# Kernel tuning notes

Hardware: AMD Instinct MI355X
Metric: run time of the kernel (lower is better)

## Reference

```python
import jax, jax.numpy as jnp
import numpy as np

# dims
BS = 4096
MOVE = 4
N_EN, ED = 64, 16
N_AL, AD = 63, 16
OTHER = 20
MF = MOVE + OTHER            # m_f_size = 24
IN = MOVE + N_EN * ED + N_AL * AD + OTHER  # 2056
H = 4                        # n_head
HE = 128                     # hypernet_emb
E = 64                       # attention_dim (emb_dim)
NA = N_EN + N_AL + 1         # n_agents = 128
RNN = 256
EN_START = MOVE
AL_START = MOVE + N_EN * ED
OTH_START = AL_START + N_AL * AD


def setup_inputs() -> dict:
    key = jax.random.key(0)
    ks = jax.random.split(key, 32)
    g = lambda k, shape: (jax.random.normal(k, shape, dtype=jnp.float32) * 0.05)
    return {
        "obs": jax.random.normal(ks[0], (BS, IN), dtype=jnp.float32),
        # per-head query MLP (Linear(MF,HE)+ReLU+Linear(HE,E,no bias)), stacked over heads
        "Wq1": g(ks[1], (H, HE, MF)), "bq1": g(ks[2], (H, HE)), "Wq2": g(ks[3], (H, E, HE)),
        # per-head key_m MLP
        "Wkm1": g(ks[4], (H, HE, MF)), "bkm1": g(ks[5], (H, HE)), "Wkm2": g(ks[6], (H, E, HE)),
        # per-head entity key linears (no bias)
        "Wke": g(ks[7], (H, E, ED)), "Wka": g(ks[8], (H, E, AD)),
        # per-head value_m MLP
        "Wvm1": g(ks[9], (H, HE, MF)), "bvm1": g(ks[10], (H, HE)), "Wvm2": g(ks[11], (H, E, HE)),
        # per-head entity value linears (no bias)
        "Wve": g(ks[12], (H, E, ED)), "Wva": g(ks[13], (H, E, AD)),
        # b net: Linear(IN,E)+ReLU+Linear(E,1)
        "Wb1": g(ks[14], (E, IN)), "bb1": g(ks[15], (E,)), "Wb2": g(ks[16], (1, E)), "bb2": g(ks[17], (1,)),
        # hyper_w_head: Linear(IN,HE)+ReLU+Linear(HE,H)
        "Wh1": g(ks[18], (HE, IN)), "bh1": g(ks[19], (HE,)), "Wh2": g(ks[20], (H, HE)), "bh2": g(ks[21], (H,)),
        # final layer: Linear(E*NA, RNN)
        "Wf": g(ks[22], (RNN, E * NA)), "bf": g(ks[23], (RNN,)),
    }


def _headed_mlp(x, W1, b1, W2):
    # x: [B, MF]; W1: [H, HE, MF]; W2: [H, E, HE] -> [B, H, E]
    h = jax.nn.relu(jnp.einsum("bf,hgf->bhg", x, W1) + b1[None])
    return jnp.einsum("bhg,heg->bhe", h, W2)


def reference(obs, Wq1, bq1, Wq2, Wkm1, bkm1, Wkm2, Wke, Wka,
              Wvm1, bvm1, Wvm2, Wve, Wva, Wb1, bb1, Wb2, bb2,
              Wh1, bh1, Wh2, bh2, Wf, bf):
    bs = obs.shape[0]
    m = jnp.concatenate([obs[:, :MOVE], obs[:, OTH_START:]], axis=1)        # [B, MF]
    enemies = obs[:, EN_START:AL_START].reshape(bs, N_EN, ED)               # [B, N_EN, ED]
    allies = obs[:, AL_START:OTH_START].reshape(bs, N_AL, AD)               # [B, N_AL, AD]

    q = _headed_mlp(m, Wq1, bq1, Wq2)                                       # [B, H, E]
    km = _headed_mlp(m, Wkm1, bkm1, Wkm2)[:, :, None, :]                    # [B, H, 1, E]
    ke = jnp.einsum("bnd,hed->bhne", enemies, Wke)                          # [B, H, N_EN, E]
    ka = jnp.einsum("bnd,hed->bhne", allies, Wka)                           # [B, H, N_AL, E]
    k = jnp.concatenate([km, ke, ka], axis=2)                               # [B, H, NA, E]

    vm = _headed_mlp(m, Wvm1, bvm1, Wvm2)[:, :, None, :]
    ve = jnp.einsum("bnd,hed->bhne", enemies, Wve)
    va = jnp.einsum("bnd,hed->bhne", allies, Wva)
    v = jnp.concatenate([vm, ve, va], axis=2)                               # [B, H, NA, E]

    logits = jnp.einsum("bhe,bhne->bhn", q, k) / np.sqrt(E).astype(np.float32)
    w = jax.nn.softmax(logits, axis=-1)                                     # [B, H, NA]
    # torch: atten_w (B,1,NA) expanded to (B,E,NA) * v permuted to (B,E,NA); flatten [E,NA]
    scores = (w[:, :, None, :] * jnp.swapaxes(v, 2, 3)).reshape(bs, H, E * NA)

    b_term = jax.nn.relu(obs @ Wb1.T + bb1) @ Wb2.T + bb2                   # [B, 1]
    w_head = jnp.abs(jax.nn.relu(obs @ Wh1.T + bh1) @ Wh2.T + bh2)          # [B, H]
    mixed = jnp.einsum("bhk,bh->bk", scores, w_head) + b_term               # [B, E*NA]
    return mixed @ Wf.T + bf                                                # [B, RNN]
```

## Files before the change

kernel.cpp:

```cpp
#include <hip/hip_runtime.h>
#include <hip/hip_bf16.h>

typedef __attribute__((ext_vector_type(8))) short short8;
typedef __attribute__((ext_vector_type(4))) float floatx4;

#define NIN 2056
#define KPAD 2080
#define NBS 4096

__device__ __forceinline__ void gl_lds16(const ushort* g, ushort* l) {
#if defined(__has_builtin) && __has_builtin(__builtin_amdgcn_global_load_lds)
  __builtin_amdgcn_global_load_lds(
      (const __attribute__((address_space(1))) unsigned int*)g,
      (__attribute__((address_space(3))) unsigned int*)l, 16, 0, 0);
#else
  *(uint4*)l = *(const uint4*)g;
#endif
}

__device__ __forceinline__ float wsum(float v) {
#pragma unroll
  for (int o = 32; o; o >>= 1) v += __shfl_xor(v, o, 64);
  return v;
}
__device__ __forceinline__ float wmax(float v) {
#pragma unroll
  for (int o = 32; o; o >>= 1) v = fmaxf(v, __shfl_xor(v, o, 64));
  return v;
}

__global__ void prep_small(const float* __restrict__ obs,
                           const float* __restrict__ Wb1, const float* __restrict__ Wh1,
                           const float* __restrict__ Wq1, const float* __restrict__ Wkm1,
                           const float* __restrict__ Wvm1, const float* __restrict__ bq1,
                           const float* __restrict__ bkm1, const float* __restrict__ bvm1,
                           const float* __restrict__ Wq2, const float* __restrict__ Wkm2,
                           const float* __restrict__ Wvm2,
                           __hip_bfloat16* __restrict__ mmat,
                           __hip_bfloat16* __restrict__ w1cat,
                           __hip_bfloat16* __restrict__ w1m, float* __restrict__ b1cat,
                           __hip_bfloat16* __restrict__ w2cat) {
  int bid = blockIdx.x, tid = threadIdx.x;
  if (bid < 512) {
    int idx = bid * 256 + tid;
    int b = idx >> 5, j = idx & 31;
    float v = 0.f;
    if (j < 4) v = obs[(size_t)b * NIN + j];
    else if (j < 24) v = obs[(size_t)b * NIN + 2032 + j];
    mmat[idx] = __float2bfloat16(v);
  } else if (bid < 704) {
    int r = bid - 512;
    const float* src = (r < 64) ? (Wb1 + (size_t)r * NIN) : (Wh1 + (size_t)(r - 64) * NIN);
    for (int j = tid; j < KPAD; j += 256)
      w1cat[(size_t)r * KPAD + j] = __float2bfloat16(j < NIN ? src[j] : 0.f);
  } else if (bid < 896) {
    int idx = (bid - 704) * 256 + tid;
    int row = idx >> 5, j = idx & 31;
    int net = row >> 9, hg = row & 511;
    const float* W1 = net == 0 ? Wq1 : (net == 1 ? Wkm1 : Wvm1);
    float v = (j < 24) ? W1[(size_t)hg * 24 + j] : 0.f;
    w1m[idx] = __float2bfloat16(v);
    if (j == 0) {
      const float* b1 = net == 0 ? bq1 : (net == 1 ? bkm1 : bvm1);
      b1cat[row] = b1[hg];
    }
  } else {
    int idx = (bid - 896) * 256 + tid;
    int row = idx >> 7, g = idx & 127;
    int net = row >> 8, he = row & 255;
    const float* W2 = net == 0 ? Wq2 : (net == 1 ? Wkm2 : Wvm2);
    w2cat[idx] = __float2bfloat16(W2[(size_t)he * 128 + g]);
  }
}

__global__ void p6a_twf(const float* __restrict__ Wf, float* __restrict__ Wft,
                        float* __restrict__ rowsum) {
  __shared__ float t[64][65];
  int kt = blockIdx.x, rt = blockIdx.y;
  int tid = threadIdx.x;
  int kl = tid & 63, r0 = tid >> 6;
#pragma unroll
  for (int ii = 0; ii < 16; ++ii) {
    int rl = ii * 4 + r0;
    t[rl][kl] = Wf[(size_t)(rt * 64 + rl) * 8192 + kt * 64 + kl];
  }
  __syncthreads();
#pragma unroll
  for (int ii = 0; ii < 16; ++ii) {
    int kl2 = ii * 4 + r0;
    Wft[(size_t)(kt * 64 + kl2) * 256 + rt * 64 + kl] = t[kl][kl2];
  }
  if (tid < 64) {
    float s = 0.f;
    for (int kk = 0; kk < 64; ++kk) s += t[tid][kk];
    atomicAdd(&rowsum[rt * 64 + tid], s);
  }
}

__global__ void p6b_yt(const float* __restrict__ Wft, const float* __restrict__ Wve,
                       const float* __restrict__ Wva, __hip_bfloat16* __restrict__ Yt) {
  int n = blockIdx.x;
  int r = threadIdx.x;
  if (n == 0) {
    alignas(16) __hip_bfloat16 tmp[8];
    for (int e0 = 0; e0 < 64; e0 += 8) {
#pragma unroll
      for (int j = 0; j < 8; ++j)
        tmp[j] = __float2bfloat16(Wft[(size_t)((e0 + j) * 128) * 256 + r]);
      *(uint4*)(Yt + (size_t)r * 8192 + 8128 + e0) = *(const uint4*)tmp;
    }
    return;
  }
  const float* Wv = (n <= 64) ? Wve : Wva;
  float accv[64];
#pragma unroll
  for (int j = 0; j < 64; ++j) accv[j] = 0.f;
  for (int e = 0; e < 64; ++e) {
    float v = Wft[(size_t)(e * 128 + n) * 256 + r];
#pragma unroll
    for (int hd = 0; hd < 64; ++hd)
      accv[hd] += Wv[(hd >> 4) * 1024 + e * 16 + (hd & 15)] * v;
  }
#pragma unroll
  for (int c = 0; c < 8; ++c) {
    alignas(16) __hip_bfloat16 tmp[8];
#pragma unroll
    for (int j = 0; j < 8; ++j) tmp[j] = __float2bfloat16(accv[c * 8 + j]);
    *(uint4*)(Yt + (size_t)r * 8192 + (n - 1) * 64 + c * 8) = *(const uint4*)tmp;
  }
}

template <bool BIAS_RELU_BF16>
__global__ __launch_bounds__(256) void gemm64(
    const __hip_bfloat16* __restrict__ A, int lda, long aZ,
    const __hip_bfloat16* __restrict__ B, int ldb, long bZ,
    float* __restrict__ Cf, __hip_bfloat16* __restrict__ Cb, int ldc, long cZ,
    int nK, const float* __restrict__ bias) {
  __shared__ alignas(16) ushort lA[64 * 40];
  __shared__ alignas(16) ushort lB[64 * 40];
  int mt = blockIdx.x, nt = blockIdx.y, z = blockIdx.z;
  const ushort* Ag = (const ushort*)A + (size_t)z * aZ + (size_t)mt * 64 * lda;
  const ushort* Bg = (const ushort*)B + (size_t)z * bZ + (size_t)nt * 64 * ldb;
  int t = threadIdx.x;
  int w = t >> 6, l = t & 63, r16 = l & 15, kg = l >> 4;
  int srow = t >> 2, skc = (t & 3) * 8;
  const ushort* ga = Ag + (size_t)srow * lda + skc;
  const ushort* gb = Bg + (size_t)srow * ldb + skc;
  ushort* sa = lA + srow * 40 + skc;
  ushort* sb = lB + srow * 40 + skc;
  const ushort* fa = lA + (w * 16 + r16) * 40 + kg * 8;
  const ushort* fb0 = lB + r16 * 40 + kg * 8;
  floatx4 zero4 = {0.f, 0.f, 0.f, 0.f};
  floatx4 acc[4] = {zero4, zero4, zero4, zero4};
  for (int ks = 0; ks < nK; ++ks) {
    uint4 va = *(const uint4*)(ga + ks * 32);
    uint4 vb = *(const uint4*)(gb + ks * 32);
    __syncthreads();
    *(uint4*)sa = va;
    *(uint4*)sb = vb;
    __syncthreads();
    short8 a = *(const short8*)fa;
#pragma unroll
    for (int c = 0; c < 4; ++c) {
      short8 bb = *(const short8*)(fb0 + c * 16 * 40);
      acc[c] = __builtin_amdgcn_mfma_f32_16x16x32_bf16(a, bb, acc[c], 0, 0, 0);
    }
  }
  int row0 = mt * 64 + w * 16 + kg * 4;
  int col0 = nt * 64 + r16;
#pragma unroll
  for (int c = 0; c < 4; ++c) {
    int col = col0 + c * 16;
#pragma unroll
    for (int r = 0; r < 4; ++r) {
      int row = row0 + r;
      float v = acc[c][r];
      if (BIAS_RELU_BF16) {
        v += bias[col];
        v = v > 0.f ? v : 0.f;
        Cb[(size_t)z * cZ + (size_t)row * ldc + col] = __float2bfloat16(v);
      } else {
        Cf[(size_t)z * cZ + (size_t)row * ldc + col] = v;
      }
    }
  }
}

__global__ __launch_bounds__(256) void gemm_h1(
    const float* __restrict__ obs, const __hip_bfloat16* __restrict__ w1cat_,
    float* __restrict__ H1p) {
  __shared__ alignas(16) ushort lA[64 * 40];
  __shared__ alignas(16) ushort lB[64 * 40];
  const ushort* w1cat = (const ushort*)w1cat_;
  int mt = blockIdx.x, nt = blockIdx.y, z = blockIdx.z;
  int t = threadIdx.x;
  int w = t >> 6, l = t & 63, r16 = l & 15, kg = l >> 4;
  int srow = t >> 2, sc = (t & 3) * 8;
  int k0 = z * 512;
  const float* ga = obs + (size_t)(mt * 64 + srow) * NIN + k0 + sc;
  const ushort* gb = w1cat + (size_t)(nt * 64 + srow) * KPAD + k0 + sc;
  ushort* sa = lA + srow * 40 + sc;
  ushort* sb = lB + srow * 40 + sc;
  const ushort* fa = lA + (w * 16 + r16) * 40 + kg * 8;
  const ushort* fb0 = lB + r16 * 40 + kg * 8;
  floatx4 zero4 = {0.f, 0.f, 0.f, 0.f};
  floatx4 acc[4] = {zero4, zero4, zero4, zero4};
  int nK = (z == 3) ? 17 : 16;
  for (int ks = 0; ks < nK; ++ks) {
    float4 f0, f1;
    uint4 vb;
    bool tail = (ks == 16);
    if (!tail || (t & 3) == 0) {
      f0 = *(const float4*)(ga + ks * 32);
      f1 = *(const float4*)(ga + ks * 32 + 4);
    } else {
      f0 = make_float4(0.f, 0.f, 0.f, 0.f);
      f1 = make_float4(0.f, 0.f, 0.f, 0.f);
    }
    vb = *(const uint4*)(gb + ks * 32);
    __syncthreads();
    alignas(16) __hip_bfloat16 tmp[8];
    tmp[0] = __float2bfloat16(f0.x); tmp[1] = __float2bfloat16(f0.y);
    tmp[2] = __float2bfloat16(f0.z); tmp[3] = __float2bfloat16(f0.w);
    tmp[4] = __float2bfloat16(f1.x); tmp[5] = __float2bfloat16(f1.y);
    tmp[6] = __float2bfloat16(f1.z); tmp[7] = __float2bfloat16(f1.w);
    *(uint4*)sa = *(const uint4*)tmp;
    *(uint4*)sb = vb;
    __syncthreads();
    short8 a = *(const short8*)fa;
#pragma unroll
    for (int c = 0; c < 4; ++c) {
      short8 bb = *(const short8*)(fb0 + c * 16 * 40);
      acc[c] = __builtin_amdgcn_mfma_f32_16x16x32_bf16(a, bb, acc[c], 0, 0, 0);
    }
  }
  int row0 = mt * 64 + w * 16 + kg * 4;
  int col0 = nt * 64 + r16;
  float* C = H1p + (size_t)z * NBS * 192;
#pragma unroll
  for (int c = 0; c < 4; ++c)
#pragma unroll
    for (int r = 0; r < 4; ++r)
      C[(size_t)(row0 + r) * 192 + col0 + c * 16] = acc[c][r];
}

__global__ __launch_bounds__(256) void gemm_final(
    const ushort* __restrict__ Xg, const ushort* __restrict__ Yt,
    float* __restrict__ part) {
  __shared__ alignas(16) ushort lA[128 * 32];
  __shared__ alignas(16) ushort lB[128 * 32];
  int bid = blockIdx.x;
  int z = bid & 7, nt = (bid >> 3) & 1, mt = bid >> 4;
  int t = threadIdx.x;
  int w = t >> 6, l = t & 63, r16 = l & 15, kg = l >> 4;
  int wr = (w >> 1) * 64, wc = (w & 1) * 64;
  const ushort* ga0 = Xg + (size_t)(mt * 128 + (t >> 2)) * 8192 + z * 1024 + (t & 3) * 8;
  const ushort* ga1 = ga0 + (size_t)64 * 8192;
  const ushort* gb0 = Yt + (size_t)(nt * 128 + (t >> 2)) * 8192 + z * 1024 + (t & 3) * 8;
  const ushort* gb1 = gb0 + (size_t)64 * 8192;
  ushort* la0 = lA + t * 8;
  ushort* la1 = lA + 2048 + t * 8;
  ushort* lb0 = lB + t * 8;
  ushort* lb1 = lB + 2048 + t * 8;
  const ushort* fa0 = lA + (wr + r16) * 32 + kg * 8;
  const ushort* fb0 = lB + (wc + r16) * 32 + kg * 8;
  floatx4 zero4 = {0.f, 0.f, 0.f, 0.f};
  floatx4 acc[4][4];
#pragma unroll
  for (int i = 0; i < 4; ++i)
#pragma unroll
    for (int j = 0; j < 4; ++j) acc[i][j] = zero4;
  for (int ks = 0; ks < 32; ++ks) {
    gl_lds16(ga0, la0);
    gl_lds16(ga1, la1);
    gl_lds16(gb0, lb0);
    gl_lds16(gb1, lb1);
    ga0 += 32; ga1 += 32; gb0 += 32; gb1 += 32;
    __syncthreads();
    short8 a[4], b[4];
#pragma unroll
    for (int mi = 0; mi < 4; ++mi) a[mi] = *(const short8*)(fa0 + mi * 512);
#pragma unroll
    for (int ni = 0; ni < 4; ++ni) b[ni] = *(const short8*)(fb0 + ni * 512);
#pragma unroll
    for (int mi = 0; mi < 4; ++mi)
#pragma unroll
      for (int ni = 0; ni < 4; ++ni)
        acc[mi][ni] = __builtin_amdgcn_mfma_f32_16x16x32_bf16(a[mi], b[ni], acc[mi][ni], 0, 0, 0);
    __syncthreads();
  }
  int row0 = mt * 128 + wr + kg * 4;
  int col0 = nt * 128 + wc + r16;
  float* cp = part + (size_t)z * NBS * 256;
#pragma unroll
  for (int mi = 0; mi < 4; ++mi)
#pragma unroll
    for (int ni = 0; ni < 4; ++ni)
#pragma unroll
      for (int r = 0; r < 4; ++r)
        cp[(size_t)(row0 + mi * 16 + r) * 256 + col0 + ni * 16] = acc[mi][ni][r];
}

__global__ __launch_bounds__(64) void row_kernel(
    const float* __restrict__ obs, const float* __restrict__ QKV,
    const float* __restrict__ H1p, const float* __restrict__ Wke,
    const float* __restrict__ Wka, const float* __restrict__ Wb2,
    const float* __restrict__ bb2, const float* __restrict__ Wh2,
    const float* __restrict__ bh2, const float* __restrict__ bb1,
    const float* __restrict__ bh1, __hip_bfloat16* __restrict__ X,
    float* __restrict__ bterm) {
  __shared__ float q_lds[256];
  __shared__ float qke_lds[64], qka_lds[64];
  int b = blockIdx.x;
  int lane = threadIdx.x;
  const float* qkv = QKV + (size_t)b * 768;
  float q_h[4], km_h[4], vm_h[4];
#pragma unroll
  for (int h = 0; h < 4; ++h) {
    q_h[h] = qkv[h * 64 + lane];
    km_h[h] = qkv[256 + h * 64 + lane];
    vm_h[h] = qkv[512 + h * 64 + lane];
    q_lds[h * 64 + lane] = q_h[h];
  }
  __syncthreads();
  {
    int h = lane >> 4, d = lane & 15;
    float se = 0.f, sa = 0.f;
    for (int e = 0; e < 64; ++e) {
      float qv = q_lds[h * 64 + e];
      se += qv * Wke[h * 1024 + e * 16 + d];
      sa += qv * Wka[h * 1024 + e * 16 + d];
    }
    qke_lds[lane] = se;
    qka_lds[lane] = sa;
  }
  __syncthreads();
  float l0[4];
#pragma unroll
  for (int h = 0; h < 4; ++h) l0[h] = wsum(q_h[h] * km_h[h]) * 0.125f;
  const float* ob = obs + (size_t)b * NIN;
  alignas(16) float en[16];
  alignas(16) float al[16];
  {
    const float4* ep = (const float4*)(ob + 4 + lane * 16);
    const float4* ap = (const float4*)(ob + 1028 + lane * 16);
#pragma unroll
    for (int i = 0; i < 4; ++i) {
      *(float4*)(en + 4 * i) = ep[i];
      *(float4*)(al + 4 * i) = ap[i];
    }
  }
  bool av = lane < 63;
  float lE[4], lA_[4];
#pragma unroll
  for (int h = 0; h < 4; ++h) {
    float sE = 0.f, sA = 0.f;
#pragma unroll
    for (int d = 0; d < 16; ++d) {
      sE += en[d] * qke_lds[h * 16 + d];
      sA += al[d] * qka_lds[h * 16 + d];
    }
    lE[h] = sE * 0.125f;
    lA_[h] = sA * 0.125f;
  }
  const float* h1p = H1p + (size_t)b * 192;
  const size_t S1 = (size_t)NBS * 192;
  float vb0 = h1p[lane] + h1p[S1 + lane] + h1p[2 * S1 + lane] + h1p[3 * S1 + lane];
  float vw0 = h1p[64 + lane] + h1p[S1 + 64 + lane] + h1p[2 * S1 + 64 + lane] + h1p[3 * S1 + 64 + lane];
  float vw1 = h1p[128 + lane] + h1p[S1 + 128 + lane] + h1p[2 * S1 + 128 + lane] + h1p[3 * S1 + 128 + lane];
  float hb = fmaxf(vb0 + bb1[lane], 0.f);
  float bt = wsum(hb * Wb2[lane]) + bb2[0];
  float hw0 = fmaxf(vw0 + bh1[lane], 0.f);
  float hw1 = fmaxf(vw1 + bh1[64 + lane], 0.f);
  float whead[4];
#pragma unroll
  for (int h = 0; h < 4; ++h)
    whead[h] = fabsf(wsum(hw0 * Wh2[h * 128 + lane] + hw1 * Wh2[h * 128 + 64 + lane]) + bh2[h]);
  float wE[4], wA[4], w0[4];
#pragma unroll
  for (int h = 0; h < 4; ++h) {
    float mE = wmax(lE[h]);
    float mA = wmax(av ? lA_[h] : -3.0e38f);
    float mx = fmaxf(fmaxf(mE, mA), l0[h]);
    float pE = __expf(lE[h] - mx);
    float pA = av ? __expf(lA_[h] - mx) : 0.f;
    float p0 = __expf(l0[h] - mx);
    float den = wsum(pE + pA) + p0;
    float s = whead[h] / den;
    wE[h] = pE * s;
    wA[h] = pA * s;
    w0[h] = p0 * s;
  }
  __hip_bfloat16* xr = X + (size_t)b * 8192;
#pragma unroll
  for (int h = 0; h < 4; ++h) {
    alignas(16) __hip_bfloat16 tmp[16];
#pragma unroll
    for (int d = 0; d < 16; ++d) tmp[d] = __float2bfloat16(wE[h] * en[d]);
    uint4* dst = (uint4*)(xr + (size_t)lane * 64 + h * 16);
    dst[0] = ((const uint4*)tmp)[0];
    dst[1] = ((const uint4*)tmp)[1];
  }
  if (av) {
#pragma unroll
    for (int h = 0; h < 4; ++h) {
      alignas(16) __hip_bfloat16 tmp[16];
#pragma unroll
      for (int d = 0; d < 16; ++d) tmp[d] = __float2bfloat16(wA[h] * al[d]);
      uint4* dst = (uint4*)(xr + (size_t)(64 + lane) * 64 + h * 16);
      dst[0] = ((const uint4*)tmp)[0];
      dst[1] = ((const uint4*)tmp)[1];
    }
  }
  float x0 = w0[0] * vm_h[0] + w0[1] * vm_h[1] + w0[2] * vm_h[2] + w0[3] * vm_h[3];
  xr[8128 + lane] = __float2bfloat16(x0);
  if (lane == 0) bterm[b] = bt;
}

__global__ void k7_out(const float* __restrict__ part, const float* __restrict__ bterm,
                       const float* __restrict__ rowsum, const float* __restrict__ bfv,
                       float* __restrict__ out) {
  int b = blockIdx.x, r = threadIdx.x;
  size_t i = (size_t)b * 256 + r;
  const size_t S = (size_t)NBS * 256;
  float v = 0.f;
#pragma unroll
  for (int z = 0; z < 8; ++z) v += part[i + z * S];
  out[i] = v + bterm[b] * rowsum[r] + bfv[r];
}

extern "C" void kernel_launch(void* const* d_in, const int* in_sizes, int n_in,
                              void* d_out, int out_size, void* d_ws, size_t ws_size,
                              hipStream_t stream) {
  const float* obs = (const float*)d_in[0];
  const float* Wq1 = (const float*)d_in[1];
  const float* bq1 = (const float*)d_in[2];
  const float* Wq2 = (const float*)d_in[3];
  const float* Wkm1 = (const float*)d_in[4];
  const float* bkm1 = (const float*)d_in[5];
  const float* Wkm2 = (const float*)d_in[6];
  const float* Wke = (const float*)d_in[7];
  const float* Wka = (const float*)d_in[8];
  const float* Wvm1 = (const float*)d_in[9];
  const float* bvm1 = (const float*)d_in[10];
  const float* Wvm2 = (const float*)d_in[11];
  const float* Wve = (const float*)d_in[12];
  const float* Wva = (const float*)d_in[13];
  const float* Wb1 = (const float*)d_in[14];
  const float* bb1 = (const float*)d_in[15];
  const float* Wb2 = (const float*)d_in[16];
  const float* bb2 = (const float*)d_in[17];
  const float* Wh1 = (const float*)d_in[18];
  const float* bh1 = (const float*)d_in[19];
  const float* Wh2 = (const float*)d_in[20];
  const float* bh2 = (const float*)d_in[21];
  const float* Wf = (const float*)d_in[22];
  const float* bfv = (const float*)d_in[23];
  float* out = (float*)d_out;

  char* ws = (char*)d_ws;
  size_t off = 0;
  auto alloc = [&](size_t bytes) -> void* {
    void* p = ws + off;
    off += (bytes + 255) & ~(size_t)255;
    return p;
  };
  __hip_bfloat16* mmat = (__hip_bfloat16*)alloc((size_t)NBS * 32 * 2);
  __hip_bfloat16* w1m = (__hip_bfloat16*)alloc((size_t)1536 * 32 * 2);
  float* b1cat = (float*)alloc(1536 * 4);
  __hip_bfloat16* w2cat = (__hip_bfloat16*)alloc((size_t)768 * 128 * 2);
  __hip_bfloat16* w1cat = (__hip_bfloat16*)alloc((size_t)192 * KPAD * 2);
  float* rowsum = (float*)alloc(256 * 4);
  float* bterm = (float*)alloc(NBS * 4);
  float* Wft = (float*)alloc((size_t)8192 * 256 * 4);
  __hip_bfloat16* Yt = (__hip_bfloat16*)alloc((size_t)256 * 8192 * 2);
  __hip_bfloat16* X = (__hip_bfloat16*)alloc((size_t)NBS * 8192 * 2);
  char* R = (char*)alloc((size_t)36 * 1024 * 1024 + (size_t)2 * 1024 * 1024);
  __hip_bfloat16* HID = (__hip_bfloat16*)R;
  float* QKV = (float*)(R + (size_t)NBS * 1536 * 2);
  float* H1p = (float*)(R + (size_t)NBS * 1536 * 2 + (size_t)NBS * 768 * 4);
  float* part8 = (float*)R;

  hipMemsetAsync(rowsum, 0, 256 * 4, stream);

  prep_small<<<1280, 256, 0, stream>>>(obs, Wb1, Wh1, Wq1, Wkm1, Wvm1, bq1, bkm1, bvm1,
                                       Wq2, Wkm2, Wvm2, mmat, w1cat, w1m, b1cat, w2cat);
  p6a_twf<<<dim3(128, 4), 256, 0, stream>>>(Wf, Wft, rowsum);
  p6b_yt<<<128, 256, 0, stream>>>(Wft, Wve, Wva, Yt);

  gemm_h1<<<dim3(64, 3, 4), 256, 0, stream>>>(obs, w1cat, H1p);
  gemm64<true><<<dim3(64, 24, 1), 256, 0, stream>>>(
      mmat, 32, 0, w1m, 32, 0, nullptr, HID, 1536, 0, 1, b1cat);
  gemm64<false><<<dim3(64, 1, 12), 256, 0, stream>>>(
      HID, 1536, 128, w2cat, 128, 64 * 128, QKV, nullptr, 768, 64, 4, nullptr);
  row_kernel<<<NBS, 64, 0, stream>>>(obs, QKV, H1p, Wke, Wka, Wb2, bb2, Wh2, bh2,
                                     bb1, bh1, X, bterm);
  gemm_final<<<512, 256, 0, stream>>>((const ushort*)X, (const ushort*)Yt, part8);
  k7_out<<<NBS, 256, 0, stream>>>(part8, bterm, rowsum, bfv, out);

  (void)in_sizes; (void)n_in; (void)out_size; (void)ws_size;
}
```

Before: 270.7 us.

## Fuse two-layer headed MLP GEMMs into one kernel and pack rows per block

Replaces the two generic gemm64 launches (hidden layer with bias+ReLU to bf16 global buffer, then per-head second layer) with a single qkv_fused kernel that keeps the 64x128 hidden tile in LDS and feeds it directly into the second MFMA stage, eliminating the HID global round trip and one launch. The row_kernel now processes four batch rows per 256-thread block instead of one row per 64-thread block, reducing block count and scheduling overhead. The fused kernel reads operands straight from global without LDS staging for the first layer.

```diff
diff --git a/kernel.cpp b/kernel.cpp
--- a/kernel.cpp
+++ b/kernel.cpp
@@ -130,60 +130,54 @@
   }
 }
 
-template <bool BIAS_RELU_BF16>
-__global__ __launch_bounds__(256) void gemm64(
-    const __hip_bfloat16* __restrict__ A, int lda, long aZ,
-    const __hip_bfloat16* __restrict__ B, int ldb, long bZ,
-    float* __restrict__ Cf, __hip_bfloat16* __restrict__ Cb, int ldc, long cZ,
-    int nK, const float* __restrict__ bias) {
-  __shared__ alignas(16) ushort lA[64 * 40];
-  __shared__ alignas(16) ushort lB[64 * 40];
-  int mt = blockIdx.x, nt = blockIdx.y, z = blockIdx.z;
-  const ushort* Ag = (const ushort*)A + (size_t)z * aZ + (size_t)mt * 64 * lda;
-  const ushort* Bg = (const ushort*)B + (size_t)z * bZ + (size_t)nt * 64 * ldb;
+__global__ __launch_bounds__(256) void qkv_fused(
+    const __hip_bfloat16* __restrict__ mmat_, const __hip_bfloat16* __restrict__ w1m_,
+    const float* __restrict__ b1cat, const __hip_bfloat16* __restrict__ w2cat_,
+    float* __restrict__ QKV) {
+  __shared__ alignas(16) ushort lH[64 * 136];
+  const ushort* mmat = (const ushort*)mmat_;
+  const ushort* w1m = (const ushort*)w1m_;
+  const ushort* w2cat = (const ushort*)w2cat_;
+  int mt = blockIdx.x, z = blockIdx.y;
   int t = threadIdx.x;
   int w = t >> 6, l = t & 63, r16 = l & 15, kg = l >> 4;
-  int srow = t >> 2, skc = (t & 3) * 8;
-  const ushort* ga = Ag + (size_t)srow * lda + skc;
-  const ushort* gb = Bg + (size_t)srow * ldb + skc;
-  ushort* sa = lA + srow * 40 + skc;
-  ushort* sb = lB + srow * 40 + skc;
-  const ushort* fa = lA + (w * 16 + r16) * 40 + kg * 8;
-  const ushort* fb0 = lB + r16 * 40 + kg * 8;
   floatx4 zero4 = {0.f, 0.f, 0.f, 0.f};
-  floatx4 acc[4] = {zero4, zero4, zero4, zero4};
-  for (int ks = 0; ks < nK; ++ks) {
-    uint4 va = *(const uint4*)(ga + ks * 32);
-    uint4 vb = *(const uint4*)(gb + ks * 32);
-    __syncthreads();
-    *(uint4*)sa = va;
-    *(uint4*)sb = vb;
-    __syncthreads();
-    short8 a = *(const short8*)fa;
+  short8 a1 = *(const short8*)(mmat + (size_t)(mt * 64 + w * 16 + r16) * 32 + kg * 8);
+  floatx4 acc1[8];
+#pragma unroll
+  for (int c = 0; c < 8; ++c) {
+    short8 b1 = *(const short8*)(w1m + (size_t)(z * 128 + c * 16 + r16) * 32 + kg * 8);
+    acc1[c] = __builtin_amdgcn_mfma_f32_16x16x32_bf16(a1, b1, zero4, 0, 0, 0);
+  }
+#pragma unroll
+  for (int c = 0; c < 8; ++c) {
+    int col = c * 16 + r16;
+    float bias = b1cat[z * 128 + col];
+#pragma unroll
+    for (int r = 0; r < 4; ++r) {
+      float v = acc1[c][r] + bias;
+      v = v > 0.f ? v : 0.f;
+      __hip_bfloat16 bv = __float2bfloat16(v);
+      lH[(w * 16 + kg * 4 + r) * 136 + col] = *(ushort*)&bv;
+    }
+  }
+  __syncthreads();
+  floatx4 acc2[4] = {zero4, zero4, zero4, zero4};
+#pragma unroll
+  for (int ks = 0; ks < 4; ++ks) {
+    short8 a = *(const short8*)(lH + (w * 16 + r16) * 136 + ks * 32 + kg * 8);
 #pragma unroll
     for (int c = 0; c < 4; ++c) {
-      short8 bb = *(const short8*)(fb0 + c * 16 * 40);
-      acc[c] = __builtin_amdgcn_mfma_f32_16x16x32_bf16(a, bb, acc[c], 0, 0, 0);
-    }
-  }
-  int row0 = mt * 64 + w * 16 + kg * 4;
-  int col0 = nt * 64 + r16;
-#pragma unroll
-  for (int c = 0; c < 4; ++c) {
-    int col = col0 + c * 16;
-#pragma unroll
-    for (int r = 0; r < 4; ++r) {
-      int row = row0 + r;
-      float v = acc[c][r];
-      if (BIAS_RELU_BF16) {
-        v += bias[col];
-        v = v > 0.f ? v : 0.f;
-        Cb[(size_t)z * cZ + (size_t)row * ldc + col] = __float2bfloat16(v);
-      } else {
-        Cf[(size_t)z * cZ + (size_t)row * ldc + col] = v;
-      }
-    }
-  }
+      short8 b = *(const short8*)(w2cat + (size_t)(z * 64 + c * 16 + r16) * 128 + ks * 32 + kg * 8);
+      acc2[c] = __builtin_amdgcn_mfma_f32_16x16x32_bf16(a, b, acc2[c], 0, 0, 0);
+    }
+  }
+  float* Q = QKV + (size_t)(mt * 64) * 768 + z * 64;
+#pragma unroll
+  for (int c = 0; c < 4; ++c)
+#pragma unroll
+    for (int r = 0; r < 4; ++r)
+      Q[(size_t)(w * 16 + kg * 4 + r) * 768 + c * 16 + r16] = acc2[c][r];
 }
 
 __global__ __launch_bounds__(256) void gemm_h1(
@@ -301,7 +295,7 @@
         cp[(size_t)(row0 + mi * 16 + r) * 256 + col0 + ni * 16] = acc[mi][ni][r];
 }
 
-__global__ __launch_bounds__(64) void row_kernel(
+__global__ __launch_bounds__(256) void row_kernel(
     const float* __restrict__ obs, const float* __restrict__ QKV,
     const float* __restrict__ H1p, const float* __restrict__ Wke,
     const float* __restrict__ Wka, const float* __restrict__ Wb2,
@@ -309,10 +303,11 @@
     const float* __restrict__ bh2, const float* __restrict__ bb1,
     const float* __restrict__ bh1, __hip_bfloat16* __restrict__ X,
     float* __restrict__ bterm) {
-  __shared__ float q_lds[256];
-  __shared__ float qke_lds[64], qka_lds[64];
-  int b = blockIdx.x;
-  int lane = threadIdx.x;
+  __shared__ float q_lds[4][256];
+  __shared__ float qke_lds[4][64], qka_lds[4][64];
+  int wv = threadIdx.x >> 6;
+  int lane = threadIdx.x & 63;
+  int b = blockIdx.x * 4 + wv;
   const float* qkv = QKV + (size_t)b * 768;
   float q_h[4], km_h[4], vm_h[4];
 #pragma unroll
@@ -320,19 +315,19 @@
     q_h[h] = qkv[h * 64 + lane];
     km_h[h] = qkv[256 + h * 64 + lane];
     vm_h[h] = qkv[512 + h * 64 + lane];
-    q_lds[h * 64 + lane] = q_h[h];
+    q_lds[wv][h * 64 + lane] = q_h[h];
   }
   __syncthreads();
   {
     int h = lane >> 4, d = lane & 15;
     float se = 0.f, sa = 0.f;
     for (int e = 0; e < 64; ++e) {
-      float qv = q_lds[h * 64 + e];
+      float qv = q_lds[wv][h * 64 + e];
       se += qv * Wke[h * 1024 + e * 16 + d];
       sa += qv * Wka[h * 1024 + e * 16 + d];
     }
-    qke_lds[lane] = se;
-    qka_lds[lane] = sa;
+    qke_lds[wv][lane] = se;
+    qka_lds[wv][lane] = sa;
   }
   __syncthreads();
   float l0[4];
@@ -357,8 +352,8 @@
     float sE = 0.f, sA = 0.f;
 #pragma unroll
     for (int d = 0; d < 16; ++d) {
-      sE += en[d] * qke_lds[h * 16 + d];
-      sA += al[d] * qka_lds[h * 16 + d];
+      sE += en[d] * qke_lds[wv][h * 16 + d];
+      sA += al[d] * qka_lds[wv][h * 16 + d];
     }
     lE[h] = sE * 0.125f;
     lA_[h] = sA * 0.125f;
@@ -475,10 +470,9 @@
   float* Wft = (float*)alloc((size_t)8192 * 256 * 4);
   __hip_bfloat16* Yt = (__hip_bfloat16*)alloc((size_t)256 * 8192 * 2);
   __hip_bfloat16* X = (__hip_bfloat16*)alloc((size_t)NBS * 8192 * 2);
-  char* R = (char*)alloc((size_t)36 * 1024 * 1024 + (size_t)2 * 1024 * 1024);
-  __hip_bfloat16* HID = (__hip_bfloat16*)R;
-  float* QKV = (float*)(R + (size_t)NBS * 1536 * 2);
-  float* H1p = (float*)(R + (size_t)NBS * 1536 * 2 + (size_t)NBS * 768 * 4);
+  char* R = (char*)alloc((size_t)34 * 1024 * 1024);
+  float* QKV = (float*)R;
+  float* H1p = (float*)(R + (size_t)NBS * 768 * 4);
   float* part8 = (float*)R;
 
   hipMemsetAsync(rowsum, 0, 256 * 4, stream);
@@ -489,12 +483,9 @@
   p6b_yt<<<128, 256, 0, stream>>>(Wft, Wve, Wva, Yt);
 
   gemm_h1<<<dim3(64, 3, 4), 256, 0, stream>>>(obs, w1cat, H1p);
-  gemm64<true><<<dim3(64, 24, 1), 256, 0, stream>>>(
-      mmat, 32, 0, w1m, 32, 0, nullptr, HID, 1536, 0, 1, b1cat);
-  gemm64<false><<<dim3(64, 1, 12), 256, 0, stream>>>(
-      HID, 1536, 128, w2cat, 128, 64 * 128, QKV, nullptr, 768, 64, 4, nullptr);
-  row_kernel<<<NBS, 64, 0, stream>>>(obs, QKV, H1p, Wke, Wka, Wb2, bb2, Wh2, bh2,
-                                     bb1, bh1, X, bterm);
+  qkv_fused<<<dim3(64, 12), 256, 0, stream>>>(mmat, w1m, b1cat, w2cat, QKV);
+  row_kernel<<<NBS / 4, 256, 0, stream>>>(obs, QKV, H1p, Wke, Wka, Wb2, bb2, Wh2, bh2,
+                                          bb1, bh1, X, bterm);
   gemm_final<<<512, 256, 0, stream>>>((const ushort*)X, (const ushort*)Yt, part8);
   k7_out<<<NBS, 256, 0, stream>>>(part8, bterm, rowsum, bfv, out);
 
```

After: 271.1 us. Within noise of the previous version (+0.2%).
